# Performance work log

Measured on AMD Instinct MI355X. Metric: run time of the kernel, lower is better.

Reference implementation:

```python
import jax, jax.numpy as jnp
import numpy as np

GROUPS = 32
EPS = 1e-5
NUM_HEADS = 16


def group_norm(x, gamma, beta):
    # x: [b, c, s]; GroupNorm over (c//G, s) per group, affine per channel
    b, c, s = x.shape
    xg = x.reshape(b, GROUPS, (c // GROUPS) * s)
    mean = xg.mean(axis=-1, keepdims=True)
    var = xg.var(axis=-1, keepdims=True)
    xn = ((xg - mean) * jax.lax.rsqrt(var + EPS)).reshape(b, c, s)
    return xn * gamma[None, :, None] + beta[None, :, None]


def setup_inputs() -> dict:
    key = jax.random.key(0)
    ks = jax.random.split(key, 8)
    b, c, H, W = 16, 1024, 32, 32
    ctx_dim, Sk = 2048, 256
    x = jax.random.normal(ks[0], (b, c, H, W), jnp.float32)
    context = jax.random.normal(ks[1], (b, Sk, ctx_dim), jnp.float32)
    mask = jax.random.randint(ks[2], (b, Sk), 0, 2, jnp.int32)
    gamma_x = jnp.ones((c,), jnp.float32)
    beta_x = jnp.zeros((c,), jnp.float32)
    gamma_c = jnp.ones((ctx_dim,), jnp.float32)
    beta_c = jnp.zeros((ctx_dim,), jnp.float32)
    Wq = jax.random.normal(ks[3], (c, c), jnp.float32) * (1.0 / np.sqrt(c))
    bq = jnp.zeros((c,), jnp.float32)
    Wkv = jax.random.normal(ks[4], (2 * c, ctx_dim), jnp.float32) * (1.0 / np.sqrt(ctx_dim))
    bkv = jnp.zeros((2 * c,), jnp.float32)
    # proj_out is zero-initialized in the original (zero_module); use small random
    # weights so the attention path contributes to the output / gradients.
    Wp = jax.random.normal(ks[5], (c, c), jnp.float32) * (0.02 / np.sqrt(c))
    bp = jnp.zeros((c,), jnp.float32)
    return {"x": x, "context": context, "mask": mask,
            "gamma_x": gamma_x, "beta_x": beta_x, "gamma_c": gamma_c, "beta_c": beta_c,
            "Wq": Wq, "bq": bq, "Wkv": Wkv, "bkv": bkv, "Wp": Wp, "bp": bp}


def reference(x, context, mask, gamma_x, beta_x, gamma_c, beta_c, Wq, bq, Wkv, bkv, Wp, bp):
    b, c = x.shape[0], x.shape[1]
    spatial = x.shape[2:]
    xf = x.reshape(b, c, -1)                       # [b, c, Sq]
    Sq = xf.shape[-1]
    h_heads = NUM_HEADS
    d = c // h_heads

    # q = conv1x1(GroupNorm(x))
    q = jnp.einsum('oc,bcs->bos', Wq, group_norm(xf, gamma_x, beta_x)) + bq[None, :, None]
    # context -> [b, ctx_dim, Sk], GroupNorm, kv conv1x1
    ctx = jnp.transpose(context, (0, 2, 1))
    ctx_n = group_norm(ctx, gamma_c, beta_c)
    kv = jnp.einsum('oc,bcs->bos', Wkv, ctx_n) + bkv[None, :, None]  # [b, 2c, Sk]
    k, v = kv[:, :c], kv[:, c:]

    # QKVStableMaskedAttention: scale q and k each by 1/sqrt(sqrt(d))
    scale = 1.0 / np.sqrt(np.sqrt(d))
    qh = (q * scale).reshape(b, h_heads, d, Sq)
    kh = (k * scale).reshape(b, h_heads, d, -1)
    vh = v.reshape(b, h_heads, d, -1)
    w = jnp.einsum('bhdt,bhds->bhts', qh, kh)      # [b, h, Sq, Sk]
    mbool = mask.astype(bool)[:, None, None, :]
    w = jnp.where(mbool, w, jnp.float32(-1e9))
    w = jax.nn.softmax(w, axis=-1)                 # stable softmax (max-subtracted)
    a = jnp.einsum('bhts,bhds->bhdt', w, vh).reshape(b, c, Sq)

    h_out = jnp.einsum('oc,bcs->bos', Wp, a) + bp[None, :, None]
    return (xf + h_out).reshape(b, c, *spatial)
```

## Files before the change

kernel.cpp:

```cpp
#include <hip/hip_runtime.h>
#include <stdint.h>

#define DEV static __device__ __forceinline__

typedef unsigned short u16;
typedef u16  u16x8 __attribute__((ext_vector_type(8)));
typedef u16  u16x4 __attribute__((ext_vector_type(4)));
typedef float f32x4 __attribute__((ext_vector_type(4)));
typedef short s16x8 __attribute__((ext_vector_type(8)));

#define BB 16
#define CC 1024
#define SS 1024
#define CTX 2048
#define SKK 256
#define NH 16
#define HD 64
#define NG 32
#define ATT_SCALE 0.35355339059327373f

DEV u16 f2bf(float f) {
  uint32_t u = __float_as_uint(f);
  return (u16)((u + 0x7fffu + ((u >> 16) & 1u)) >> 16);
}
DEV s16x8 ld8(const u16* p) { return __builtin_bit_cast(s16x8, *(const u16x8*)p); }
DEV f32x4 zero4() { f32x4 z = {0.f, 0.f, 0.f, 0.f}; return z; }

DEV void gload_lds16(const void* g, const void* l) {
  __builtin_amdgcn_global_load_lds(
      (const __attribute__((address_space(1))) unsigned int*)(uintptr_t)g,
      (__attribute__((address_space(3))) unsigned int*)(uint32_t)(uintptr_t)l,
      16, 0, 0);
}

__global__ __launch_bounds__(256) void prep_misc(const float* __restrict__ Wq,
                                                 const float* __restrict__ Wkv,
                                                 const float* __restrict__ Wp,
                                                 const int* __restrict__ mask,
                                                 u16* __restrict__ wq_bf,
                                                 u16* __restrict__ wkv_bf,
                                                 u16* __restrict__ wp_bf,
                                                 float* __restrict__ mb) {
  const int bid = blockIdx.x, tid = threadIdx.x;
  const float* src; u16* dst; int i;
  if (bid < 1024)      { src = Wq;  dst = wq_bf;  i = bid * 256 + tid; }
  else if (bid < 5120) { src = Wkv; dst = wkv_bf; i = (bid - 1024) * 256 + tid; }
  else if (bid < 6144) { src = Wp;  dst = wp_bf;  i = (bid - 5120) * 256 + tid; }
  else {
    int j = (bid - 6144) * 256 + tid;
    mb[j] = mask[j] ? 0.f : -1e9f;
    return;
  }
  f32x4 v = ((const f32x4*)src)[i];
  u16x4 o; o[0]=f2bf(v[0]); o[1]=f2bf(v[1]); o[2]=f2bf(v[2]); o[3]=f2bf(v[3]);
  ((u16x4*)dst)[i] = o;
}

__global__ __launch_bounds__(256) void gn_stats_all(const float* __restrict__ x,
                                                    const float* __restrict__ ctx,
                                                    float* __restrict__ stx,
                                                    float* __restrict__ stc) {
  const int bid = blockIdx.x, tid = threadIdx.x;
  float s = 0.f, ss = 0.f;
  float* st; int slot; float inv_n;
  if (bid < 512) {
    const int b = bid >> 5, g = bid & 31;
    const float* p = x + ((size_t)b * CC + g * 32) * SS;
    for (int it = 0; it < 32; ++it) {
      f32x4 v = *(const f32x4*)(p + it * 1024 + tid * 4);
      s  += v[0] + v[1] + v[2] + v[3];
      ss += v[0]*v[0] + v[1]*v[1] + v[2]*v[2] + v[3]*v[3];
    }
    st = stx; slot = bid; inv_n = 1.f / 32768.f;
  } else {
    const int bid2 = bid - 512;
    const int b = bid2 >> 5, g = bid2 & 31;
    const float* p = ctx + (size_t)b * SKK * CTX + g * 64;
    const int ch = tid & 63, r0 = tid >> 6;
    for (int it = 0; it < 64; ++it) {
      float v = p[(size_t)(it * 4 + r0) * CTX + ch];
      s += v; ss += v * v;
    }
    st = stc; slot = bid2; inv_n = 1.f / 16384.f;
  }
  __shared__ float red[512];
  red[tid] = s; red[256 + tid] = ss;
  __syncthreads();
  for (int o = 128; o > 0; o >>= 1) {
    if (tid < o) { red[tid] += red[tid + o]; red[256 + tid] += red[256 + tid + o]; }
    __syncthreads();
  }
  if (tid == 0) {
    float mean = red[0] * inv_n;
    float var  = red[256] * inv_n - mean * mean;
    st[slot * 2 + 0] = mean;
    st[slot * 2 + 1] = rsqrtf(var + 1e-5f);
  }
}

__global__ __launch_bounds__(256) void gn_apply_all(const float* __restrict__ x,
                                                    const float* __restrict__ ctx,
                                                    const float* __restrict__ stx,
                                                    const float* __restrict__ stc,
                                                    const float* __restrict__ gamma_x,
                                                    const float* __restrict__ beta_x,
                                                    const float* __restrict__ gamma_c,
                                                    const float* __restrict__ beta_c,
                                                    u16* __restrict__ xnT,
                                                    u16* __restrict__ ctxn) {
  __shared__ float t[64][65];
  const int bid = blockIdx.x, tid = threadIdx.x;
  if (bid < 8192) {
    size_t i = ((size_t)bid * 256 + tid) * 4;
    int ch = (int)(i & 2047);
    int bs = (int)(i >> 11);
    int b = bs >> 8;
    int g = ch >> 6;
    float mean = stc[(b * 32 + g) * 2], rstd = stc[(b * 32 + g) * 2 + 1];
    f32x4 v  = *(const f32x4*)(ctx + i);
    f32x4 ga = *(const f32x4*)(gamma_c + ch);
    f32x4 be = *(const f32x4*)(beta_c + ch);
    u16x4 o;
    o[0] = f2bf((v[0] - mean) * rstd * ga[0] + be[0]);
    o[1] = f2bf((v[1] - mean) * rstd * ga[1] + be[1]);
    o[2] = f2bf((v[2] - mean) * rstd * ga[2] + be[2]);
    o[3] = f2bf((v[3] - mean) * rstd * ga[3] + be[3]);
    *(u16x4*)(ctxn + i) = o;
    return;
  }
  const int id2 = bid - 8192;
  const int b = id2 >> 8, c0 = ((id2 >> 4) & 15) * 64, s0 = (id2 & 15) * 64;
  const int j = tid & 63, i0 = tid >> 6;
  for (int it = 0; it < 16; ++it) {
    int i = it * 4 + i0;
    int c = c0 + i;
    int g = c >> 5;
    float mean = stx[(b * 32 + g) * 2], rstd = stx[(b * 32 + g) * 2 + 1];
    float v = x[((size_t)b * CC + c) * SS + s0 + j];
    t[i][j] = (v - mean) * rstd * gamma_x[c] + beta_x[c];
  }
  __syncthreads();
  for (int it = 0; it < 16; ++it) {
    int jj = it * 4 + i0;
    xnT[((size_t)b * SS + s0 + jj) * CC + c0 + j] = f2bf(t[j][jj]);
  }
}

template <int BM, int BN, int EPI>
__global__ __launch_bounds__(256) void gemm_bt(
    const u16* __restrict__ A, const u16* __restrict__ Bt, void* __restrict__ Cout,
    const float* __restrict__ bias, const float* __restrict__ resid,
    int K, int lda, int ldb, int ldc,
    long strideAb, long strideBb, long strideCb, int Nthresh, float scl) {
  constexpr int MF = BM / 32, NF = BN / 32;
  constexpr int ACH = BM / 16, BCH = BN / 16;
  __shared__ alignas(16) u16 lds_a[BM * 32];
  __shared__ alignas(16) u16 lds_b[BN * 32];
  const int tid = threadIdx.x, wid = tid >> 6, lane = tid & 63;
  const int wm = wid >> 1, wn = wid & 1;

  const int nwg  = gridDim.x * gridDim.y * gridDim.z;
  const int orig = blockIdx.x + gridDim.x * (blockIdx.y + gridDim.y * blockIdx.z);
  const int v    = (orig & 7) * (nwg >> 3) + (orig >> 3);
  const int gxy  = gridDim.x * gridDim.y;
  const int bz   = v / gxy;
  const int rr   = v - bz * gxy;
  const int by   = rr / gridDim.x;
  const int bx   = rr - by * gridDim.x;

  const u16* Ab = A + (long)bz * strideAb + (long)bx * BM * lda;
  const u16* Bb = Bt + (long)bz * strideBb + (long)by * BN * ldb;
  const int srow = lane >> 2, scol = (lane & 3) * 8;
  const int fr = lane & 15, fk = (lane >> 4) * 8;

  f32x4 acc[MF][NF];
#pragma unroll
  for (int m = 0; m < MF; ++m)
#pragma unroll
    for (int n = 0; n < NF; ++n) acc[m][n] = zero4();

  for (int kt = 0; kt < K; kt += 32) {
    __syncthreads();
#pragma unroll
    for (int c = 0; c < ACH / 4; ++c) {
      int ch = wid + c * 4;
      gload_lds16(Ab + (long)(ch * 16 + srow) * lda + kt + scol, &lds_a[ch * 512]);
    }
#pragma unroll
    for (int c = 0; c < BCH / 4; ++c) {
      int ch = wid + c * 4;
      gload_lds16(Bb + (long)(ch * 16 + srow) * ldb + kt + scol, &lds_b[ch * 512]);
    }
    __syncthreads();
    s16x8 af[MF], bfr[NF];
#pragma unroll
    for (int m = 0; m < MF; ++m) af[m] = ld8(&lds_a[(wm * (BM / 2) + m * 16 + fr) * 32 + fk]);
#pragma unroll
    for (int n = 0; n < NF; ++n) bfr[n] = ld8(&lds_b[(wn * (BN / 2) + n * 16 + fr) * 32 + fk]);
#pragma unroll
    for (int m = 0; m < MF; ++m)
#pragma unroll
      for (int n = 0; n < NF; ++n)
        acc[m][n] = __builtin_amdgcn_mfma_f32_16x16x32_bf16(af[m], bfr[n], acc[m][n], 0, 0, 0);
  }

  const int rowb = bx * BM + wm * (BM / 2) + ((lane >> 4) << 2);
  const int colb = by * BN + wn * (BN / 2) + fr;
#pragma unroll
  for (int m = 0; m < MF; ++m) {
#pragma unroll
    for (int n = 0; n < NF; ++n) {
      int col = colb + n * 16;
      f32x4 vv = acc[m][n];
      if constexpr (EPI == 0) {
        float bia = bias[col];
        float s = (col < Nthresh) ? scl : 1.0f;
        u16* C = (u16*)Cout + (long)bz * strideCb;
#pragma unroll
        for (int i = 0; i < 4; ++i) {
          int row = rowb + m * 16 + i;
          C[(long)row * ldc + col] = f2bf((vv[i] + bia) * s);
        }
      } else {
        float* C = (float*)Cout + (long)bz * strideCb;
        const float* R = resid + (long)bz * strideCb;
#pragma unroll
        for (int i = 0; i < 4; ++i) {
          int row = rowb + m * 16 + i;
          long idx = (long)row * ldc + col;
          C[idx] = R[idx] + vv[i] + bias[row];
        }
      }
    }
  }
}

__global__ __launch_bounds__(256) void transpose_v(const u16* __restrict__ kvt,
                                                   u16* __restrict__ v2) {
  __shared__ u16 t[64][66];
  const int b = blockIdx.z, s0 = blockIdx.y * 64, o0 = blockIdx.x * 64;
  const int tid = threadIdx.x, j = tid & 63, i0 = tid >> 6;
#pragma unroll
  for (int it = 0; it < 16; ++it) {
    int i = it * 4 + i0;
    t[i][j] = kvt[((long)b * SKK + s0 + i) * CTX + CC + o0 + j];
  }
  __syncthreads();
#pragma unroll
  for (int it = 0; it < 16; ++it) {
    int oi = it * 4 + i0;
    v2[((long)b * CC + o0 + oi) * SKK + s0 + j] = t[j][oi];
  }
}

__global__ __launch_bounds__(256) void attn_fused(const u16* __restrict__ qt,
                                                  const u16* __restrict__ kvt,
                                                  const u16* __restrict__ v2,
                                                  const float* __restrict__ mbias,
                                                  u16* __restrict__ at) {
  __shared__ alignas(16) u16 k_lds[256 * 64];
  __shared__ alignas(16) u16 v_lds[64 * 256];
  const int orig = blockIdx.x + 16 * blockIdx.y + 256 * blockIdx.z;
  const int v = (orig & 7) * 512 + (orig >> 3);
  const int bb = v >> 8, h = (v >> 4) & 15, t0 = (v & 15) * 64;

  const int tid = threadIdx.x, wid = tid >> 6, lane = tid & 63;
  const int fr = lane & 15, hi = lane >> 4;
  const int sw = fr & 7;

#pragma unroll
  for (int it = 0; it < 8; ++it) {
    int lin = (wid * 8 + it) * 1024 + lane * 16;
    int kr = lin >> 7, kc = (lin >> 4) & 7;
    gload_lds16(kvt + ((long)bb * SKK + kr) * CTX + h * HD + ((kc ^ (kr & 7)) << 3),
                (const char*)k_lds + (wid * 8 + it) * 1024);
    int vr = lin >> 9, vc = (lin >> 4) & 31;
    gload_lds16(v2 + ((long)bb * CC + h * HD + vr) * SKK + ((vc ^ (vr & 7)) << 3),
                (const char*)v_lds + (wid * 8 + it) * 1024);
  }

  const u16* qp = qt + ((long)bb * SS + t0 + wid * 16 + fr) * CC + h * HD + hi * 8;
  s16x8 aq0 = ld8(qp), aq1 = ld8(qp + 32);

  __syncthreads();

  f32x4 sc[16];
#pragma unroll
  for (int nf = 0; nf < 16; ++nf) {
    const u16* krow = k_lds + (nf * 16 + fr) * 64;
    s16x8 kb0 = ld8(krow + (((hi) ^ sw) << 3));
    s16x8 kb1 = ld8(krow + (((4 + hi) ^ sw) << 3));
    f32x4 z = zero4();
    z = __builtin_amdgcn_mfma_f32_16x16x32_bf16(aq0, kb0, z, 0, 0, 0);
    sc[nf] = __builtin_amdgcn_mfma_f32_16x16x32_bf16(aq1, kb1, z, 0, 0, 0);
  }

  __syncthreads();

  const float* mb = mbias + bb * SKK + fr;
#pragma unroll
  for (int nf = 0; nf < 16; ++nf) sc[nf] = sc[nf] + mb[nf * 16];

#pragma unroll
  for (int i = 0; i < 4; ++i) {
    float m = sc[0][i];
#pragma unroll
    for (int nf = 1; nf < 16; ++nf) m = fmaxf(m, sc[nf][i]);
#pragma unroll
    for (int d = 1; d < 16; d <<= 1) m = fmaxf(m, __shfl_xor(m, d));
    float s = 0.f;
#pragma unroll
    for (int nf = 0; nf < 16; ++nf) {
      float e = __expf(sc[nf][i] - m);
      sc[nf][i] = e; s += e;
    }
#pragma unroll
    for (int d = 1; d < 16; d <<= 1) s += __shfl_xor(s, d);
    float inv = 1.0f / s;
#pragma unroll
    for (int nf = 0; nf < 16; ++nf) sc[nf][i] *= inv;
  }

  u16* p_base = k_lds + wid * 4096;
#pragma unroll
  for (int nf = 0; nf < 16; ++nf) {
    int c = 2 * nf + (fr >> 3);
#pragma unroll
    for (int i = 0; i < 4; ++i) {
      int t = 4 * hi + i;
      p_base[t * 256 + (((c ^ (t & 7)) << 3)) + sw] = f2bf(sc[nf][i]);
    }
  }

  f32x4 ov[4];
#pragma unroll
  for (int n = 0; n < 4; ++n) ov[n] = zero4();
#pragma unroll
  for (int kk = 0; kk < 8; ++kk) {
    int c = 4 * kk + hi;
    s16x8 pa = ld8(p_base + fr * 256 + ((c ^ sw) << 3));
#pragma unroll
    for (int n = 0; n < 4; ++n) {
      int o = n * 16 + fr;
      s16x8 vb = ld8(v_lds + o * 256 + ((c ^ sw) << 3));
      ov[n] = __builtin_amdgcn_mfma_f32_16x16x32_bf16(pa, vb, ov[n], 0, 0, 0);
    }
  }

  const int rbase = hi * 4;
  u16* po = at + ((long)bb * SS + t0 + wid * 16 + rbase) * CC + h * HD + fr;
#pragma unroll
  for (int n = 0; n < 4; ++n)
#pragma unroll
    for (int i = 0; i < 4; ++i) po[(long)i * CC + n * 16] = f2bf(ov[n][i]);
}

extern "C" void kernel_launch(void* const* d_in, const int* in_sizes, int n_in,
                              void* d_out, int out_size, void* d_ws, size_t ws_size,
                              hipStream_t stream) {
  const float* x       = (const float*)d_in[0];
  const float* context = (const float*)d_in[1];
  const int*   mask    = (const int*)d_in[2];
  const float* gamma_x = (const float*)d_in[3];
  const float* beta_x  = (const float*)d_in[4];
  const float* gamma_c = (const float*)d_in[5];
  const float* beta_c  = (const float*)d_in[6];
  const float* Wq      = (const float*)d_in[7];
  const float* bq      = (const float*)d_in[8];
  const float* Wkv     = (const float*)d_in[9];
  const float* bkv     = (const float*)d_in[10];
  const float* Wp      = (const float*)d_in[11];
  const float* bp      = (const float*)d_in[12];
  float* out = (float*)d_out;

  char* w = (char*)d_ws;
  size_t off = 0;
  u16* wq_bf  = (u16*)(w + off); off += (size_t)CC * CC * 2;
  u16* wkv_bf = (u16*)(w + off); off += (size_t)CTX * CTX * 2;
  u16* wp_bf  = (u16*)(w + off); off += (size_t)CC * CC * 2;
  u16* xnT    = (u16*)(w + off); off += (size_t)BB * SS * CC * 2;
  u16* ctxn   = (u16*)(w + off); off += (size_t)BB * SKK * CTX * 2;
  u16* qt     = (u16*)(w + off); off += (size_t)BB * SS * CC * 2;
  u16* kvt    = (u16*)(w + off); off += (size_t)BB * SKK * CTX * 2;
  u16* v2     = (u16*)(w + off); off += (size_t)BB * CC * SKK * 2;
  u16* at     = (u16*)(w + off); off += (size_t)BB * SS * CC * 2;
  float* mb   = (float*)(w + off); off += (size_t)BB * SKK * 4;
  float* stx  = (float*)(w + off); off += (size_t)BB * NG * 2 * 4;
  float* stc  = (float*)(w + off); off += (size_t)BB * NG * 2 * 4;
  (void)ws_size; (void)in_sizes; (void)n_in; (void)out_size;

  prep_misc<<<6160, 256, 0, stream>>>(Wq, Wkv, Wp, mask, wq_bf, wkv_bf, wp_bf, mb);

  gn_stats_all<<<1024, 256, 0, stream>>>(x, context, stx, stc);

  gn_apply_all<<<12288, 256, 0, stream>>>(x, context, stx, stc,
                                          gamma_x, beta_x, gamma_c, beta_c,
                                          xnT, ctxn);

  gemm_bt<128, 128, 0><<<dim3(8, 8, BB), 256, 0, stream>>>(
      xnT, wq_bf, qt, bq, nullptr, CC, CC, CC, CC,
      (long)SS * CC, 0, (long)SS * CC, CC, ATT_SCALE);

  gemm_bt<128, 128, 0><<<dim3(2, 16, BB), 256, 0, stream>>>(
      ctxn, wkv_bf, kvt, bkv, nullptr, CTX, CTX, CTX, CTX,
      (long)SKK * CTX, 0, (long)SKK * CTX, CC, ATT_SCALE);

  transpose_v<<<dim3(16, 4, BB), 256, 0, stream>>>(kvt, v2);

  attn_fused<<<dim3(16, NH, BB), 256, 0, stream>>>(qt, kvt, v2, mb, at);

  gemm_bt<128, 128, 1><<<dim3(8, 8, BB), 256, 0, stream>>>(
      wp_bf, at, out, bp, x, CC, CC, CC, CC,
      0, (long)SS * CC, (long)SS * CC, 0, 1.0f);
}
```

Measured before the change: 445.8 us.

## Double-buffer GEMM LDS with XOR swizzle and merge Q/KV GEMMs into one launch

Replaces the generic GEMM with a shared core that double-buffers LDS tiles, issuing the next K-slice's global-to-LDS loads while computing the current one. It halves the barriers per K step. An XOR swizzle on the LDS column offset is meant to cut bank conflicts. The Q and KV projection GEMMs are merged into one launch, so their 1024 + 512 tiles fill the GPU together instead of running as two kernels. The cost is twice the LDS per block, which may lower occupancy, and the fused grid has two tile types with different K lengths.

```diff
diff --git a/kernel.cpp b/kernel.cpp
--- a/kernel.cpp
+++ b/kernel.cpp
@@ -146,90 +146,139 @@
   }
 }
 
-template <int BM, int BN, int EPI>
-__global__ __launch_bounds__(256) void gemm_bt(
-    const u16* __restrict__ A, const u16* __restrict__ Bt, void* __restrict__ Cout,
-    const float* __restrict__ bias, const float* __restrict__ resid,
-    int K, int lda, int ldb, int ldc,
-    long strideAb, long strideBb, long strideCb, int Nthresh, float scl) {
-  constexpr int MF = BM / 32, NF = BN / 32;
-  constexpr int ACH = BM / 16, BCH = BN / 16;
-  __shared__ alignas(16) u16 lds_a[BM * 32];
-  __shared__ alignas(16) u16 lds_b[BN * 32];
+DEV void gemm_core(const u16* __restrict__ Ab, const u16* __restrict__ Bb,
+                   int K, int ld, u16* lds, f32x4 acc[4][4], int wid, int lane) {
+  const int wm = wid >> 1, wn = wid & 1;
+  const int fr = lane & 15, hi = lane >> 4;
+  const int r0 = lane >> 2, c4 = lane & 3;
+  const int sc = (c4 ^ (r0 & 3)) << 3;
+
+  auto STAGE = [&](u16* buf, int kt) {
+#pragma unroll
+    for (int i = 0; i < 2; ++i) {
+      int ch = wid + i * 4;
+      long rbase = (long)(ch * 16 + r0);
+      gload_lds16(Ab + rbase * ld + kt + sc, buf + ch * 512);
+      gload_lds16(Bb + rbase * ld + kt + sc, buf + 4096 + ch * 512);
+    }
+  };
+  auto COMP = [&](const u16* buf) {
+    const int ko = ((hi ^ (fr & 3)) << 3);
+    s16x8 af[4], bf[4];
+#pragma unroll
+    for (int m = 0; m < 4; ++m) af[m] = ld8(buf + (wm * 64 + m * 16 + fr) * 32 + ko);
+#pragma unroll
+    for (int n = 0; n < 4; ++n) bf[n] = ld8(buf + 4096 + (wn * 64 + n * 16 + fr) * 32 + ko);
+#pragma unroll
+    for (int m = 0; m < 4; ++m)
+#pragma unroll
+      for (int n = 0; n < 4; ++n)
+        acc[m][n] = __builtin_amdgcn_mfma_f32_16x16x32_bf16(af[m], bf[n], acc[m][n], 0, 0, 0);
+  };
+
+  const int nt = K >> 5;
+  STAGE(lds, 0);
+  __syncthreads();
+  for (int t = 0; t < nt; t += 2) {
+    STAGE(lds + 8192, (t + 1) << 5);
+    COMP(lds);
+    __syncthreads();
+    if (t + 2 < nt) STAGE(lds, (t + 2) << 5);
+    COMP(lds + 8192);
+    __syncthreads();
+  }
+}
+
+__global__ __launch_bounds__(256) void gemm_qkv(
+    const u16* __restrict__ xnT, const u16* __restrict__ wq,
+    const u16* __restrict__ ctxn, const u16* __restrict__ wkv,
+    u16* __restrict__ qt, u16* __restrict__ kvt,
+    const float* __restrict__ bq, const float* __restrict__ bkv) {
+  __shared__ alignas(16) u16 lds[2 * 8192];
   const int tid = threadIdx.x, wid = tid >> 6, lane = tid & 63;
+  const int orig = blockIdx.x;
+  const int v = (orig & 7) * 192 + (orig >> 3);
+  const u16 *Ab, *Bb; u16* C; const float* bias;
+  int K, ld, ldc, bx, by;
+  if (v < 1024) {
+    int bz = v >> 6, r = v & 63; by = r >> 3; bx = r & 7;
+    Ab = xnT + (long)bz * SS * CC + (long)bx * 128 * CC;
+    Bb = wq + (long)by * 128 * CC;
+    C  = qt + (long)bz * SS * CC;
+    bias = bq; K = CC; ld = CC; ldc = CC;
+  } else {
+    int u = v - 1024;
+    int bz = u >> 5, r = u & 31; by = r >> 1; bx = r & 1;
+    Ab = ctxn + (long)bz * SKK * CTX + (long)bx * 128 * CTX;
+    Bb = wkv + (long)by * 128 * CTX;
+    C  = kvt + (long)bz * SKK * CTX;
+    bias = bkv; K = CTX; ld = CTX; ldc = CTX;
+  }
+  f32x4 acc[4][4];
+#pragma unroll
+  for (int m = 0; m < 4; ++m)
+#pragma unroll
+    for (int n = 0; n < 4; ++n) acc[m][n] = zero4();
+
+  gemm_core(Ab, Bb, K, ld, lds, acc, wid, lane);
+
   const int wm = wid >> 1, wn = wid & 1;
-
-  const int nwg  = gridDim.x * gridDim.y * gridDim.z;
-  const int orig = blockIdx.x + gridDim.x * (blockIdx.y + gridDim.y * blockIdx.z);
-  const int v    = (orig & 7) * (nwg >> 3) + (orig >> 3);
-  const int gxy  = gridDim.x * gridDim.y;
-  const int bz   = v / gxy;
-  const int rr   = v - bz * gxy;
-  const int by   = rr / gridDim.x;
-  const int bx   = rr - by * gridDim.x;
-
-  const u16* Ab = A + (long)bz * strideAb + (long)bx * BM * lda;
-  const u16* Bb = Bt + (long)bz * strideBb + (long)by * BN * ldb;
-  const int srow = lane >> 2, scol = (lane & 3) * 8;
-  const int fr = lane & 15, fk = (lane >> 4) * 8;
-
-  f32x4 acc[MF][NF];
-#pragma unroll
-  for (int m = 0; m < MF; ++m)
-#pragma unroll
-    for (int n = 0; n < NF; ++n) acc[m][n] = zero4();
-
-  for (int kt = 0; kt < K; kt += 32) {
-    __syncthreads();
-#pragma unroll
-    for (int c = 0; c < ACH / 4; ++c) {
-      int ch = wid + c * 4;
-      gload_lds16(Ab + (long)(ch * 16 + srow) * lda + kt + scol, &lds_a[ch * 512]);
-    }
-#pragma unroll
-    for (int c = 0; c < BCH / 4; ++c) {
-      int ch = wid + c * 4;
-      gload_lds16(Bb + (long)(ch * 16 + srow) * ldb + kt + scol, &lds_b[ch * 512]);
-    }
-    __syncthreads();
-    s16x8 af[MF], bfr[NF];
-#pragma unroll
-    for (int m = 0; m < MF; ++m) af[m] = ld8(&lds_a[(wm * (BM / 2) + m * 16 + fr) * 32 + fk]);
-#pragma unroll
-    for (int n = 0; n < NF; ++n) bfr[n] = ld8(&lds_b[(wn * (BN / 2) + n * 16 + fr) * 32 + fk]);
-#pragma unroll
-    for (int m = 0; m < MF; ++m)
-#pragma unroll
-      for (int n = 0; n < NF; ++n)
-        acc[m][n] = __builtin_amdgcn_mfma_f32_16x16x32_bf16(af[m], bfr[n], acc[m][n], 0, 0, 0);
-  }
-
-  const int rowb = bx * BM + wm * (BM / 2) + ((lane >> 4) << 2);
-  const int colb = by * BN + wn * (BN / 2) + fr;
-#pragma unroll
-  for (int m = 0; m < MF; ++m) {
-#pragma unroll
-    for (int n = 0; n < NF; ++n) {
+  const int fr = lane & 15, hi = lane >> 4;
+  const int rowb = bx * 128 + wm * 64 + hi * 4;
+  const int colb = by * 128 + wn * 64 + fr;
+#pragma unroll
+  for (int m = 0; m < 4; ++m) {
+#pragma unroll
+    for (int n = 0; n < 4; ++n) {
+      int col = colb + n * 16;
+      float bia = bias[col];
+      float s = (col < CC) ? ATT_SCALE : 1.0f;
+      f32x4 vv = acc[m][n];
+#pragma unroll
+      for (int i = 0; i < 4; ++i) {
+        int row = rowb + m * 16 + i;
+        C[(long)row * ldc + col] = f2bf((vv[i] + bia) * s);
+      }
+    }
+  }
+}
+
+__global__ __launch_bounds__(256) void gemm_proj(
+    const u16* __restrict__ wp, const u16* __restrict__ at,
+    float* __restrict__ out, const float* __restrict__ bp,
+    const float* __restrict__ x) {
+  __shared__ alignas(16) u16 lds[2 * 8192];
+  const int tid = threadIdx.x, wid = tid >> 6, lane = tid & 63;
+  const int orig = blockIdx.x;
+  const int v = (orig & 7) * 128 + (orig >> 3);
+  const int bz = v >> 6, r = v & 63, by = r >> 3, bx = r & 7;
+  const u16* Ab = wp + (long)bx * 128 * CC;
+  const u16* Bb = at + (long)bz * SS * CC + (long)by * 128 * CC;
+  f32x4 acc[4][4];
+#pragma unroll
+  for (int m = 0; m < 4; ++m)
+#pragma unroll
+    for (int n = 0; n < 4; ++n) acc[m][n] = zero4();
+
+  gemm_core(Ab, Bb, CC, CC, lds, acc, wid, lane);
+
+  float* C = out + (long)bz * SS * CC;
+  const float* R = x + (long)bz * SS * CC;
+  const int wm = wid >> 1, wn = wid & 1;
+  const int fr = lane & 15, hi = lane >> 4;
+  const int rowb = bx * 128 + wm * 64 + hi * 4;
+  const int colb = by * 128 + wn * 64 + fr;
+#pragma unroll
+  for (int m = 0; m < 4; ++m) {
+#pragma unroll
+    for (int n = 0; n < 4; ++n) {
       int col = colb + n * 16;
       f32x4 vv = acc[m][n];
-      if constexpr (EPI == 0) {
-        float bia = bias[col];
-        float s = (col < Nthresh) ? scl : 1.0f;
-        u16* C = (u16*)Cout + (long)bz * strideCb;
-#pragma unroll
-        for (int i = 0; i < 4; ++i) {
-          int row = rowb + m * 16 + i;
-          C[(long)row * ldc + col] = f2bf((vv[i] + bia) * s);
-        }
-      } else {
-        float* C = (float*)Cout + (long)bz * strideCb;
-        const float* R = resid + (long)bz * strideCb;
-#pragma unroll
-        for (int i = 0; i < 4; ++i) {
-          int row = rowb + m * 16 + i;
-          long idx = (long)row * ldc + col;
-          C[idx] = R[idx] + vv[i] + bias[row];
-        }
+#pragma unroll
+      for (int i = 0; i < 4; ++i) {
+        int row = rowb + m * 16 + i;
+        long idx = (long)row * CC + col;
+        C[idx] = R[idx] + vv[i] + bp[row];
       }
     }
   }
@@ -397,19 +446,11 @@
                                           gamma_x, beta_x, gamma_c, beta_c,
                                           xnT, ctxn);
 
-  gemm_bt<128, 128, 0><<<dim3(8, 8, BB), 256, 0, stream>>>(
-      xnT, wq_bf, qt, bq, nullptr, CC, CC, CC, CC,
-      (long)SS * CC, 0, (long)SS * CC, CC, ATT_SCALE);
-
-  gemm_bt<128, 128, 0><<<dim3(2, 16, BB), 256, 0, stream>>>(
-      ctxn, wkv_bf, kvt, bkv, nullptr, CTX, CTX, CTX, CTX,
-      (long)SKK * CTX, 0, (long)SKK * CTX, CC, ATT_SCALE);
+  gemm_qkv<<<1536, 256, 0, stream>>>(xnT, wq_bf, ctxn, wkv_bf, qt, kvt, bq, bkv);
 
   transpose_v<<<dim3(16, 4, BB), 256, 0, stream>>>(kvt, v2);
 
   attn_fused<<<dim3(16, NH, BB), 256, 0, stream>>>(qt, kvt, v2, mb, at);
 
-  gemm_bt<128, 128, 1><<<dim3(8, 8, BB), 256, 0, stream>>>(
-      wp_bf, at, out, bp, x, CC, CC, CC, CC,
-      0, (long)SS * CC, (long)SS * CC, 0, 1.0f);
-}
+  gemm_proj<<<1024, 256, 0, stream>>>(wp_bf, at, out, bp, x);
+}
```

Result: no change. 448.8 us (+0.7%).
